# Kernel tuning notes

Hardware: AMD Instinct MI355X
Metric: run time of the kernel (lower is better)

The kernel has to match this reference:

```python
import jax, jax.numpy as jnp
import numpy as np

D = 256      # feature_dim (d_model)
H = 4        # num_heads
N = 4096     # query nodes
M = 4096     # source nodes


def _conv1x1(W, b, x):
    # Conv1d(kernel_size=1): per-position linear over channels. x: [1, Cin, N]
    return jnp.einsum('oi,bin->bon', W, x) + b[None, :, None]


def setup_inputs() -> dict:
    key = jax.random.key(0)
    ks = jax.random.split(key, 16)
    s = 0.02
    inp = {
        'x':      jax.random.normal(ks[0], (1, D, N), jnp.float32),
        'source': jax.random.normal(ks[1], (1, D, M), jnp.float32),
        'dist':   jax.random.uniform(ks[2], (1, N, M), jnp.float32),
        'mask':   jax.random.bernoulli(ks[3], 0.5, (N, M)),
        'Wq': s * jax.random.normal(ks[4], (D, D), jnp.float32),  'bq': jnp.zeros((D,), jnp.float32),
        'Wk': s * jax.random.normal(ks[5], (D, D), jnp.float32),  'bk': jnp.zeros((D,), jnp.float32),
        'Wv': s * jax.random.normal(ks[6], (D, D), jnp.float32),  'bv': jnp.zeros((D,), jnp.float32),
        'Wm': s * jax.random.normal(ks[7], (D, D), jnp.float32),  'bm': jnp.zeros((D,), jnp.float32),
        'W1': s * jax.random.normal(ks[8], (2 * D, 2 * D), jnp.float32), 'b1': jnp.zeros((2 * D,), jnp.float32),
        'W2': s * jax.random.normal(ks[9], (D, 2 * D), jnp.float32),     'b2': jnp.zeros((D,), jnp.float32),
    }
    return inp


def reference(x, source, dist, mask, Wq, bq, Wk, bk, Wv, bv, Wm, bm, W1, b1, W2, b2):
    dim = D // H  # per-head dim; torch view(1, dim, H, -1) splits channels as (dim, H)
    q = _conv1x1(Wq, bq, x).reshape(1, dim, H, N)
    k = _conv1x1(Wk, bk, source).reshape(1, dim, H, M)
    v = _conv1x1(Wv, bv, source).reshape(1, dim, H, M)

    scores = jnp.einsum('bdhn,bdhm->bhnm', q, k) / jnp.sqrt(jnp.asarray(dim, q.dtype))
    # non-standard additive mask: global detached min scales the masked-out entries
    smin = jax.lax.stop_gradient(scores.min())
    scores = scores + smin * (~mask).astype(scores.dtype)[None, None, :, :]

    prob = jax.nn.softmax(scores, axis=-1)                       # [1,H,N,M]
    attn = jnp.einsum('bhnm,bdhm->bdhn', prob, v)                # [1,dim,H,N]
    message = _conv1x1(Wm, bm, attn.reshape(1, D, N))            # merge heads

    h = jnp.concatenate([x, message], axis=1)                    # [1,2D,N]
    h = jax.nn.relu(_conv1x1(W1, b1, h))
    y = _conv1x1(W2, b2, h)                                      # [1,D,N]
    weights = scores.mean(axis=1)                                # [1,N,M]
    return y, weights
```

## Files before the change

### kernel.cpp

```cpp
#include <hip/hip_runtime.h>
#include <hip/hip_bf16.h>
#include <math.h>

#define Dm 256
#define Hh 4
#define Nn 4096
#define Mq 4096

typedef __attribute__((ext_vector_type(8))) short bf16x8;
typedef __attribute__((ext_vector_type(4))) float f32x4;
typedef _Float16 __attribute__((ext_vector_type(4))) f16x4;
typedef __fp16 __attribute__((ext_vector_type(2))) h16x2;

#define MFMA_BF16(a,b,c) __builtin_amdgcn_mfma_f32_16x16x32_bf16(a,b,c,0,0,0)
#define MFMA_F16x16(a,b,c) __builtin_amdgcn_mfma_f32_16x16x16f16(a,b,c,0,0,0)

#define MB (1u<<20)
#define OFF_FLAG  0
#define OFF_SMIN  64
#define OFF_KMAX  128
#define OFF_PART  1024
#define OFF_MT    8192
#define OFF_DENP  (128u<<10)
#define OFF_WB    (3u*MB/2)
#define OFF_BITS  (3u*MB)
#define OFF_QB    (5u*MB)
#define OFF_KB    (7u*MB)
#define OFF_VB    (9u*MB)
#define OFF_HCAT  (11u*MB)
#define OFF_ATTNT (15u*MB)
#define OFF_XT    (17u*MB)
#define OFF_ST    (19u*MB)
#define OFF_OPART (17u*MB)
#define OFF_H1T   (17u*MB)

#define WOFF_Q  0
#define WOFF_K  65536
#define WOFF_V  131072
#define WOFF_M  196608
#define WOFF_1  262144
#define WOFF_2  524288

__device__ __forceinline__ unsigned short f2bf(float x) {
    unsigned u = __float_as_uint(x);
    u += 0x7FFF + ((u >> 16) & 1);
    return (unsigned short)(u >> 16);
}
__device__ __forceinline__ float bf2f(unsigned short b) {
    return __uint_as_float(((unsigned)b) << 16);
}

__global__ void k_detect(const unsigned char* __restrict__ mb, int* __restrict__ flag,
                         unsigned* __restrict__ kmax) {
    __shared__ int c[5];
    if (threadIdx.x < 5) c[threadIdx.x] = 0;
    if (threadIdx.x < 4) kmax[threadIdx.x] = 0u;
    __syncthreads();
    for (int i = threadIdx.x; i < 16384; i += blockDim.x) {
        unsigned char b = mb[i];
        if (b) {
            atomicAdd(&c[i & 3], 1);
            if ((i & 7) == 4) atomicAdd(&c[4], 1);
        }
    }
    __syncthreads();
    if (threadIdx.x == 0) {
        int f;
        if (c[3] > 0 && c[0] == 0)          f = 3;
        else if (c[1] | c[2] | c[3])        f = 1;
        else if (c[4] > 0)                  f = 0;
        else                                f = 2;
        *flag = f;
    }
}

__global__ void k_maskbits(const void* __restrict__ mp, const int* __restrict__ flagp,
                           unsigned char* __restrict__ bits) {
    size_t i = (size_t)blockIdx.x * 256 + threadIdx.x;
    const int flag = *flagp;
    size_t base = i * 8;
    unsigned b = 0;
    if (flag == 1) {
        unsigned long long u = *(const unsigned long long*)((const unsigned char*)mp + base);
        #pragma unroll
        for (int j = 0; j < 8; j++) b |= (unsigned)(((u >> (8*j)) & 0xFFull) != 0ull) << j;
    } else if (flag == 0) {
        const int* p = (const int*)mp;
        #pragma unroll
        for (int j = 0; j < 8; j++) b |= (unsigned)(p[base + j] != 0) << j;
    } else if (flag == 3) {
        const float* p = (const float*)mp;
        #pragma unroll
        for (int j = 0; j < 8; j++) b |= (unsigned)(p[base + j] != 0.0f) << j;
    } else {
        const unsigned long long* p = (const unsigned long long*)mp;
        #pragma unroll
        for (int j = 0; j < 8; j++) b |= (unsigned)(p[base + j] != 0ull) << j;
    }
    bits[i] = (unsigned char)b;
}

__global__ __launch_bounds__(256) void k_prep(const float* __restrict__ x,
                                              const float* __restrict__ source,
                                              unsigned short* __restrict__ xt,
                                              unsigned short* __restrict__ st,
                                              unsigned short* __restrict__ hcat) {
    const int z = blockIdx.z;
    const float* src = z ? source : x;
    unsigned short* dst = z ? st : xt;
    unsigned short* dst2 = z ? nullptr : hcat;
    const int l = threadIdx.x & 63, g = threadIdx.x >> 6;
    const int c = blockIdx.y * 64 + l;
    const int n0 = blockIdx.x * 32 + g * 8;
    float4 v0 = *(const float4*)(src + (size_t)c * Nn + n0);
    float4 v1 = *(const float4*)(src + (size_t)c * Nn + n0 + 4);
    float vv[8] = {v0.x, v0.y, v0.z, v0.w, v1.x, v1.y, v1.z, v1.w};
    #pragma unroll
    for (int j = 0; j < 8; j++) {
        unsigned short b = f2bf(vv[j]);
        dst[(size_t)(n0 + j) * 256 + c] = b;
        if (dst2) dst2[(size_t)(n0 + j) * 512 + c] = b;
    }
}

__global__ void k_wcast(const float* __restrict__ Wq, const float* __restrict__ Wk,
                        const float* __restrict__ Wv, const float* __restrict__ Wm,
                        const float* __restrict__ W1, const float* __restrict__ W2,
                        unsigned short* __restrict__ wb) {
    size_t i = (size_t)blockIdx.x * 256 + threadIdx.x;
    const float* s; size_t off;
    if      (i < 65536)               { s = Wq; off = i; }
    else if (i < 131072)              { s = Wk; off = i - 65536; }
    else if (i < 196608)              { s = Wv; off = i - 131072; }
    else if (i < 262144)              { s = Wm; off = i - 196608; }
    else if (i < 524288)              { s = W1; off = i - 262144; }
    else                              { s = W2; off = i - 524288; }
    wb[i] = f2bf(s[off]);
}

template<int KK, int JT>
__device__ __forceinline__ void gemm_body(const unsigned short* __restrict__ wb,
                                          const float* __restrict__ bias,
                                          const unsigned short* __restrict__ xt,
                                          void* __restrict__ out, int mode,
                                          int bx, int by) {
    const int tid = threadIdx.x, w = tid >> 6, lane = tid & 63;
    const int lg = lane >> 4, lr = lane & 15;
    const int o_base = by * 64 + w * 16;
    const int n_base = bx * (16 * JT);
    f32x4 acc[JT];
    #pragma unroll
    for (int j = 0; j < JT; j++) acc[j] = (f32x4){0.f, 0.f, 0.f, 0.f};
    const unsigned short* wrow = wb + (size_t)(o_base + lr) * KK + lg * 8;
    const unsigned short* xrow = xt + (size_t)(n_base + lr) * KK + lg * 8;
    #pragma unroll
    for (int k0 = 0; k0 < KK; k0 += 32) {
        bf16x8 af = *(const bf16x8*)(wrow + k0);
        #pragma unroll
        for (int j = 0; j < JT; j++) {
            bf16x8 bfr = *(const bf16x8*)(xrow + (size_t)j * 16 * KK + k0);
            acc[j] = MFMA_BF16(af, bfr, acc[j]);
        }
    }
    float bv[4];
    #pragma unroll
    for (int r = 0; r < 4; r++) bv[r] = bias[o_base + lg * 4 + r];
    #pragma unroll
    for (int j = 0; j < JT; j++) {
        #pragma unroll
        for (int r = 0; r < 4; r++) {
            int o = o_base + lg * 4 + r;
            int n = n_base + j * 16 + lr;
            float v = acc[j][r] + bv[r];
            if (mode == 0) {
                ((float*)out)[(size_t)o * Nn + n] = v;
            } else if (mode == 1) {
                ((unsigned short*)out)[(((size_t)(o & 3)) * Nn + n) * 64 + (o >> 2)] = f2bf(v);
            } else if (mode == 2) {
                union { _Float16 h; unsigned short u; } cv; cv.h = (_Float16)v;
                ((unsigned short*)out)[(((size_t)(o & 3)) * 64 + (o >> 2)) * Mq + n] = cv.u;
            } else if (mode == 3) {
                ((unsigned short*)out)[(size_t)n * 512 + 256 + o] = f2bf(v);
            } else if (mode == 4) {
                ((unsigned short*)out)[(size_t)n * 512 + o] = f2bf(fmaxf(v, 0.f));
            } else {
                int dd = o >> 2, hh = o & 3, g = dd >> 3, pos = dd & 7;
                int slot = g ^ (n & 7);
                ((unsigned short*)out)[(((size_t)hh * Mq + n)) * 64 + slot * 8 + pos] = f2bf(v);
            }
        }
    }
}

template<int KK>
__global__ __launch_bounds__(256) void k_mgemm(const unsigned short* __restrict__ wb,
                                               const float* __restrict__ bias,
                                               const unsigned short* __restrict__ xt,
                                               void* __restrict__ out, int mode) {
    gemm_body<KK, 2>(wb, bias, xt, out, mode, blockIdx.x, blockIdx.y);
}

__global__ __launch_bounds__(256) void k_qkv(const unsigned short* __restrict__ wb,
                                             const float* __restrict__ bq,
                                             const float* __restrict__ bk,
                                             const float* __restrict__ bv,
                                             const unsigned short* __restrict__ xt,
                                             const unsigned short* __restrict__ st,
                                             void* __restrict__ qb, void* __restrict__ kb,
                                             void* __restrict__ vb) {
    const int z = blockIdx.z;
    const float* bias = (z == 0) ? bq : ((z == 1) ? bk : bv);
    const unsigned short* X = (z == 0) ? xt : st;
    void* out = (z == 0) ? qb : ((z == 1) ? kb : vb);
    int mode = (z == 0) ? 1 : ((z == 1) ? 5 : 2);
    gemm_body<256, 4>(wb + z * 65536, bias, X, out, mode, blockIdx.x, blockIdx.y);
}

__global__ __launch_bounds__(256) void k_knorm(const unsigned short* __restrict__ kb,
                                               unsigned* __restrict__ kmax) {
    const int h = blockIdx.y;
    const int m = blockIdx.x * 256 + threadIdx.x;
    const unsigned short* row = kb + ((size_t)(h * Mq + m) << 6);
    float s = 0.f;
    #pragma unroll
    for (int i = 0; i < 64; i++) { float v = bf2f(row[i]); s = fmaf(v, v, s); }
    __shared__ float red[256];
    red[threadIdx.x] = s;
    __syncthreads();
    for (int st = 128; st > 0; st >>= 1) {
        if (threadIdx.x < st) red[threadIdx.x] = fmaxf(red[threadIdx.x], red[threadIdx.x + st]);
        __syncthreads();
    }
    if (threadIdx.x == 0) atomicMax(kmax + h, __float_as_uint(red[0]));
}

__global__ __launch_bounds__(256) void k_qnorm(const unsigned short* __restrict__ qb,
                                               const unsigned* __restrict__ kmax,
                                               float* __restrict__ mtarr) {
    const int row = blockIdx.x * 256 + threadIdx.x;
    const unsigned short* qr = qb + ((size_t)row << 6);
    float s = 0.f;
    #pragma unroll
    for (int i = 0; i < 64; i++) { float v = bf2f(qr[i]); s = fmaf(v, v, s); }
    float k2 = __uint_as_float(kmax[row >> 12]);
    mtarr[row] = sqrtf(s * k2) * 0.125f;
}

__global__ __launch_bounds__(256) void k_min(
    const unsigned short* __restrict__ qb, const unsigned short* __restrict__ kb,
    float* __restrict__ partial) {
    __shared__ unsigned short kbuf[2][8192];
    const int tid = threadIdx.x;
    const int w = tid >> 6, lane = tid & 63;
    const int lg = lane >> 4, lr = lane & 15;
    const int n0 = blockIdx.x * 128 + w * 32;
    const int m0 = blockIdx.y * 256;

    bf16x8 qf[4][2][2];
    #pragma unroll
    for (int h = 0; h < 4; h++)
        #pragma unroll
        for (int ns = 0; ns < 2; ns++)
            #pragma unroll
            for (int kh = 0; kh < 2; kh++)
                qf[h][ns][kh] = *(const bf16x8*)(qb + (((size_t)h * Nn + n0 + ns*16 + lr) << 6) + kh*32 + lg*8);

    const unsigned short* srcs[4];
    #pragma unroll
    for (int h = 0; h < 4; h++) srcs[h] = kb + (((size_t)h * Mq + m0) << 6) + tid * 8;

    float mn = INFINITY;

    bf16x8 r[4];
    #pragma unroll
    for (int h = 0; h < 4; h++) {
        r[h] = *(const bf16x8*)(srcs[h]);
        *(bf16x8*)&kbuf[0][h * 2048 + tid * 8] = r[h];
    }
    __syncthreads();
    #pragma unroll
    for (int h = 0; h < 4; h++) r[h] = *(const bf16x8*)(srcs[h] + 2048);

    for (int t = 0; t < 8; t++) {
        const unsigned short* kB = &kbuf[t & 1][0];
        #pragma unroll
        for (int mi = 0; mi < 2; mi++) {
            const int rowoff = (mi * 16 + lr) * 64;
            #pragma unroll
            for (int h = 0; h < 4; h++) {
                bf16x8 a0 = *(const bf16x8*)(kB + h*2048 + rowoff + ((lg ^ (lr & 7)) << 3));
                bf16x8 a1 = *(const bf16x8*)(kB + h*2048 + rowoff + (((lg + 4) ^ (lr & 7)) << 3));
                #pragma unroll
                for (int ns = 0; ns < 2; ns++) {
                    f32x4 acc = (f32x4){0.f, 0.f, 0.f, 0.f};
                    acc = MFMA_BF16(a0, qf[h][ns][0], acc);
                    acc = MFMA_BF16(a1, qf[h][ns][1], acc);
                    mn = fminf(mn, fminf(fminf(acc[0], acc[1]), fminf(acc[2], acc[3])));
                }
            }
        }
        if (t < 7) {
            #pragma unroll
            for (int h = 0; h < 4; h++)
                *(bf16x8*)&kbuf[(t + 1) & 1][h * 2048 + tid * 8] = r[h];
        }
        __syncthreads();
        if (t < 6) {
            #pragma unroll
            for (int h = 0; h < 4; h++) r[h] = *(const bf16x8*)(srcs[h] + (size_t)(t + 2) * 2048);
        }
    }

    for (int off = 1; off < 64; off <<= 1) mn = fminf(mn, __shfl_xor(mn, off));
    __shared__ float wmin[4];
    if (lane == 0) wmin[w] = mn;
    __syncthreads();
    if (tid == 0) {
        float m2 = fminf(fminf(wmin[0], wmin[1]), fminf(wmin[2], wmin[3]));
        partial[blockIdx.x * 16 + blockIdx.y] = m2 * 0.125f;
    }
}

__global__ void k_minreduce(const float* __restrict__ partial, float* __restrict__ smin) {
    const int tid = threadIdx.x;
    float mn = fminf(partial[tid], partial[tid + 256]);
    __shared__ float red[256];
    red[tid] = mn;
    __syncthreads();
    for (int st = 128; st > 0; st >>= 1) {
        if (tid < st) red[tid] = fminf(red[tid], red[tid + st]);
        __syncthreads();
    }
    if (tid == 0) *smin = red[0];
}

__global__ __launch_bounds__(256) void k_wout(
    const unsigned short* __restrict__ qb, const unsigned short* __restrict__ kb,
    const unsigned long long* __restrict__ bits,
    const float* __restrict__ sminp, float* __restrict__ wout) {
    __shared__ unsigned short kbuf[2][8192];
    const int tid = threadIdx.x;
    const int w = tid >> 6, lane = tid & 63;
    const int lg = lane >> 4, lr = lane & 15;
    const int n0 = blockIdx.x * 128 + w * 32;
    const int m0 = blockIdx.y * 256;
    const float smin = *sminp;

    bf16x8 qf[4][2][2];
    #pragma unroll
    for (int h = 0; h < 4; h++)
        #pragma unroll
        for (int ns = 0; ns < 2; ns++)
            #pragma unroll
            for (int kh = 0; kh < 2; kh++)
                qf[h][ns][kh] = *(const bf16x8*)(qb + (((size_t)h * Nn + n0 + ns*16 + lr) << 6) + kh*32 + lg*8);

    const unsigned short* srcs[4];
    #pragma unroll
    for (int h = 0; h < 4; h++) srcs[h] = kb + (((size_t)h * Mq + m0) << 6) + tid * 8;

    const unsigned long long* brow0 = bits + (((size_t)(n0 + lr)) << 6) + (m0 >> 6);
    const unsigned long long* brow1 = bits + (((size_t)(n0 + 16 + lr)) << 6) + (m0 >> 6);
    unsigned long long bw0 = 0ull, bw1 = 0ull;

    bf16x8 r[4];
    #pragma unroll
    for (int h = 0; h < 4; h++) {
        r[h] = *(const bf16x8*)(srcs[h]);
        *(bf16x8*)&kbuf[0][h * 2048 + tid * 8] = r[h];
    }
    __syncthreads();
    #pragma unroll
    for (int h = 0; h < 4; h++) r[h] = *(const bf16x8*)(srcs[h] + 2048);

    for (int t = 0; t < 8; t++) {
        const unsigned short* kB = &kbuf[t & 1][0];
        const int mch = m0 + t * 32;
        if ((t & 1) == 0) { bw0 = brow0[t >> 1]; bw1 = brow1[t >> 1]; }
        #pragma unroll
        for (int mi = 0; mi < 2; mi++) {
            const int rowoff = (mi * 16 + lr) * 64;
            f32x4 acc[2][2];
            #pragma unroll
            for (int ns = 0; ns < 2; ns++) {
                acc[ns][0] = (f32x4){0.f, 0.f, 0.f, 0.f};
                acc[ns][1] = (f32x4){0.f, 0.f, 0.f, 0.f};
            }
            #pragma unroll
            for (int h = 0; h < 4; h++) {
                bf16x8 a0 = *(const bf16x8*)(kB + h*2048 + rowoff + ((lg ^ (lr & 7)) << 3));
                bf16x8 a1 = *(const bf16x8*)(kB + h*2048 + rowoff + (((lg + 4) ^ (lr & 7)) << 3));
                const int hf = h >> 1;
                #pragma unroll
                for (int ns = 0; ns < 2; ns++) {
                    acc[ns][hf] = MFMA_BF16(a0, qf[h][ns][0], acc[ns][hf]);
                    acc[ns][hf] = MFMA_BF16(a1, qf[h][ns][1], acc[ns][hf]);
                }
            }
            const int shb = (t & 1) * 32 + mi * 16 + lg * 4;
            #pragma unroll
            for (int ns = 0; ns < 2; ns++) {
                unsigned long long bw = ns ? bw1 : bw0;
                f32x4 wv;
                #pragma unroll
                for (int rr = 0; rr < 4; rr++) {
                    bool b = (bw >> (shb + rr)) & 1ull;
                    wv[rr] = fmaf(acc[ns][0][rr] + acc[ns][1][rr], 0.03125f, b ? 0.f : smin);
                }
                __builtin_nontemporal_store(wv,
                    (f32x4*)(wout + (size_t)(n0 + ns*16 + lr) * Mq + mch + mi * 16 + lg * 4));
            }
        }
        if (t < 7) {
            #pragma unroll
            for (int h = 0; h < 4; h++)
                *(bf16x8*)&kbuf[(t + 1) & 1][h * 2048 + tid * 8] = r[h];
        }
        __syncthreads();
        if (t < 6) {
            #pragma unroll
            for (int h = 0; h < 4; h++) r[h] = *(const bf16x8*)(srcs[h] + (size_t)(t + 2) * 2048);
        }
    }
}

__global__ __launch_bounds__(256) void k_pv(
    const unsigned short* __restrict__ qb, const unsigned short* __restrict__ kb,
    const unsigned short* __restrict__ vbh,
    const unsigned long long* __restrict__ bits,
    const float* __restrict__ sminp, const float* __restrict__ mtarr,
    float* __restrict__ denp, unsigned short* __restrict__ opart) {
    __shared__ unsigned short kbuf[2][4096];
    __shared__ unsigned short vbuf[2][4096];
    const int tid = threadIdx.x;
    const int w = tid >> 6, lane = tid & 63;
    const int lg = lane >> 4, lr = lane & 15;
    const int h = blockIdx.y & 3, mb = blockIdx.y >> 2;
    const int n0 = blockIdx.x * 128 + w * 32;
    const int m0 = mb * 1024;
    const float smin = *sminp;
    const float sminc = fmaxf(smin, 0.f);

    bf16x8 qf[2][2];
    float cT[2], cF[2];
    #pragma unroll
    for (int ns = 0; ns < 2; ns++) {
        const size_t qrow = ((size_t)h * Nn + n0 + ns*16 + lr) << 6;
        qf[ns][0] = *(const bf16x8*)(qb + qrow + lg*8);
        qf[ns][1] = *(const bf16x8*)(qb + qrow + 32 + lg*8);
        float mtE = mtarr[(size_t)h * Nn + n0 + ns*16 + lr] + sminc;
        cT[ns] = -mtE * 1.44269504f;
        cF[ns] = cT[ns] + smin * 1.44269504f;
    }

    f32x4 oacc[2][4];
    #pragma unroll
    for (int ns = 0; ns < 2; ns++)
        #pragma unroll
        for (int ds = 0; ds < 4; ds++) oacc[ns][ds] = (f32x4){0.f, 0.f, 0.f, 0.f};
    float dsum[2] = {0.f, 0.f};

    const unsigned short* ksrc = kb + (((size_t)h * Mq + m0) << 6) + tid * 8;
    const int vj = tid & 7;
    const int vdd0 = tid >> 3, vdd1 = 32 + (tid >> 3);
    const unsigned short* vsrc0 = vbh + (size_t)(h * 64 + vdd0) * Mq + m0 + vj * 8;
    const unsigned short* vsrc1 = vbh + (size_t)(h * 64 + vdd1) * Mq + m0 + vj * 8;
    int vdstA, vdstB, vdstC, vdstD;
    {
        int vds = vdd0 >> 4, vlr = vdd0 & 15, vmi = vj >> 1;
        int vswz = (vlr >> 2) & 3;
        int vbase = ((vmi * 4 + vds) * 16 + vlr) * 4;
        vdstA = (vbase + (((vj & 1) * 2 + 0) ^ vswz)) * 4;
        vdstB = (vbase + (((vj & 1) * 2 + 1) ^ vswz)) * 4;
        vds = vdd1 >> 4; vlr = vdd1 & 15;
        vswz = (vlr >> 2) & 3;
        vbase = ((vmi * 4 + vds) * 16 + vlr) * 4;
        vdstC = (vbase + (((vj & 1) * 2 + 0) ^ vswz)) * 4;
        vdstD = (vbase + (((vj & 1) * 2 + 1) ^ vswz)) * 4;
    }

    union U8 { bf16x8 v; unsigned long long q[2]; };
    U8 rv0, rv1;
    bf16x8 rk0 = *(const bf16x8*)(ksrc);
    bf16x8 rk1 = *(const bf16x8*)(ksrc + 2048);
    rv0.v = *(const bf16x8*)(vsrc0);
    rv1.v = *(const bf16x8*)(vsrc1);
    *(bf16x8*)&kbuf[0][tid * 8] = rk0;
    *(bf16x8*)&kbuf[0][2048 + tid * 8] = rk1;
    *(unsigned long long*)&vbuf[0][vdstA] = rv0.q[0];
    *(unsigned long long*)&vbuf[0][vdstB] = rv0.q[1];
    *(unsigned long long*)&vbuf[0][vdstC] = rv1.q[0];
    *(unsigned long long*)&vbuf[0][vdstD] = rv1.q[1];
    __syncthreads();
    rk0 = *(const bf16x8*)(ksrc + 4096);
    rk1 = *(const bf16x8*)(ksrc + 4096 + 2048);
    rv0.v = *(const bf16x8*)(vsrc0 + 64);
    rv1.v = *(const bf16x8*)(vsrc1 + 64);

    const unsigned long long* brow0 = bits + (((size_t)(n0 + lr)) << 6) + (m0 >> 6);
    const unsigned long long* brow1 = bits + (((size_t)(n0 + 16 + lr)) << 6) + (m0 >> 6);
    const int kslot0 = (lg ^ (lr & 7)) << 3;
    const int kslot1 = ((lg + 4) ^ (lr & 7)) << 3;
    const int vrslot = (lg ^ ((lr >> 2) & 3)) * 4;

    for (int t = 0; t < 16; t++) {
        const unsigned short* kB = &kbuf[t & 1][0];
        const unsigned short* vB = &vbuf[t & 1][0];
        unsigned long long bw[2];
        bw[0] = brow0[t];
        bw[1] = brow1[t];
        #pragma unroll
        for (int mi = 0; mi < 4; mi++) {
            const int rowoff = (mi * 16 + lr) * 64;
            bf16x8 a0 = *(const bf16x8*)(kB + rowoff + kslot0);
            bf16x8 a1 = *(const bf16x8*)(kB + rowoff + kslot1);
            f16x4 vf[4];
            #pragma unroll
            for (int ds = 0; ds < 4; ds++)
                vf[ds] = *(const f16x4*)&vB[((mi * 4 + ds) * 16 + lr) * 16 + vrslot];
            const int shb = mi * 16 + lg * 4;
            #pragma unroll
            for (int ns = 0; ns < 2; ns++) {
                f32x4 acc = (f32x4){0.f, 0.f, 0.f, 0.f};
                acc = MFMA_BF16(a0, qf[ns][0], acc);
                acc = MFMA_BF16(a1, qf[ns][1], acc);
                float p0 = exp2f(fmaf(acc[0], 0.18033688f, ((bw[ns] >> (shb + 0)) & 1ull) ? cT[ns] : cF[ns]));
                float p1 = exp2f(fmaf(acc[1], 0.18033688f, ((bw[ns] >> (shb + 1)) & 1ull) ? cT[ns] : cF[ns]));
                float p2 = exp2f(fmaf(acc[2], 0.18033688f, ((bw[ns] >> (shb + 2)) & 1ull) ? cT[ns] : cF[ns]));
                float p3 = exp2f(fmaf(acc[3], 0.18033688f, ((bw[ns] >> (shb + 3)) & 1ull) ? cT[ns] : cF[ns]));
                dsum[ns] += (p0 + p1) + (p2 + p3);
                union { h16x2 h2[2]; f16x4 f4; } pu;
                pu.h2[0] = __builtin_amdgcn_cvt_pkrtz(p0, p1);
                pu.h2[1] = __builtin_amdgcn_cvt_pkrtz(p2, p3);
                f16x4 pf = pu.f4;
                #pragma unroll
                for (int ds = 0; ds < 4; ds++)
                    oacc[ns][ds] = MFMA_F16x16(pf, vf[ds], oacc[ns][ds]);
            }
        }
        if (t < 15) {
            *(bf16x8*)&kbuf[(t + 1) & 1][tid * 8] = rk0;
            *(bf16x8*)&kbuf[(t + 1) & 1][2048 + tid * 8] = rk1;
            *(unsigned long long*)&vbuf[(t + 1) & 1][vdstA] = rv0.q[0];
            *(unsigned long long*)&vbuf[(t + 1) & 1][vdstB] = rv0.q[1];
            *(unsigned long long*)&vbuf[(t + 1) & 1][vdstC] = rv1.q[0];
            *(unsigned long long*)&vbuf[(t + 1) & 1][vdstD] = rv1.q[1];
        }
        __syncthreads();
        if (t < 14) {
            rk0 = *(const bf16x8*)(ksrc + (size_t)(t + 2) * 4096);
            rk1 = *(const bf16x8*)(ksrc + (size_t)(t + 2) * 4096 + 2048);
            rv0.v = *(const bf16x8*)(vsrc0 + (size_t)(t + 2) * 64);
            rv1.v = *(const bf16x8*)(vsrc1 + (size_t)(t + 2) * 64);
        }
    }

    #pragma unroll
    for (int ns = 0; ns < 2; ns++) {
        dsum[ns] += __shfl_xor(dsum[ns], 16);
        dsum[ns] += __shfl_xor(dsum[ns], 32);
    }
    if (lane < 16) {
        #pragma unroll
        for (int ns = 0; ns < 2; ns++)
            denp[((size_t)h * Nn + n0 + ns*16 + lane) * 4 + mb] = dsum[ns];
    }

    unsigned short* op = opart + (size_t)mb * (Dm * Nn);
    #pragma unroll
    for (int ns = 0; ns < 2; ns++)
        #pragma unroll
        for (int ds = 0; ds < 4; ds++) {
            int c = (ds * 16 + lr) * 4 + h;
            int n = n0 + ns * 16 + lg * 4;
            unsigned long long pk =
                (unsigned long long)f2bf(oacc[ns][ds][0]) |
                ((unsigned long long)f2bf(oacc[ns][ds][1]) << 16) |
                ((unsigned long long)f2bf(oacc[ns][ds][2]) << 32) |
                ((unsigned long long)f2bf(oacc[ns][ds][3]) << 48);
            *(unsigned long long*)&op[(size_t)c * Nn + n] = pk;
        }
}

__global__ __launch_bounds__(256) void k_finish(const unsigned short* __restrict__ opart,
                                                const float* __restrict__ denp,
                                                unsigned short* __restrict__ attnT) {
    __shared__ float t[64][65];
    const int cb = blockIdx.y * 64, nb = blockIdx.x * 64;
    const int tid = threadIdx.x;
    #pragma unroll
    for (int e = 0; e < 16; e++) {
        int idx = e * 256 + tid;
        int c_l = idx >> 6, n_l = idx & 63;
        int c = cb + c_l, n = nb + n_l;
        float s = 0.f;
        #pragma unroll
        for (int y = 0; y < 4; y++)
            s += bf2f(opart[(size_t)y * (Dm*Nn) + (size_t)c * Nn + n]);
        size_t row = (size_t)(c & 3) * Nn + n;
        float d = denp[row*4] + denp[row*4+1] + denp[row*4+2] + denp[row*4+3];
        t[c_l][n_l] = s / d;
    }
    __syncthreads();
    #pragma unroll
    for (int e = 0; e < 16; e++) {
        int idx = e * 256 + tid;
        int n_l = idx >> 6, c_l = idx & 63;
        attnT[(size_t)(nb + n_l) * 256 + cb + c_l] = f2bf(t[c_l][n_l]);
    }
}

extern "C" void kernel_launch(void* const* d_in, const int* in_sizes, int n_in,
                              void* d_out, int out_size, void* d_ws, size_t ws_size,
                              hipStream_t stream) {
    const float* x      = (const float*)d_in[0];
    const float* source = (const float*)d_in[1];
    const void*  mask   = d_in[3];
    const float* Wq = (const float*)d_in[4];  const float* bq = (const float*)d_in[5];
    const float* Wk = (const float*)d_in[6];  const float* bk = (const float*)d_in[7];
    const float* Wv = (const float*)d_in[8];  const float* bv = (const float*)d_in[9];
    const float* Wm = (const float*)d_in[10]; const float* bm = (const float*)d_in[11];
    const float* W1 = (const float*)d_in[12]; const float* b1 = (const float*)d_in[13];
    const float* W2 = (const float*)d_in[14]; const float* b2 = (const float*)d_in[15];

    float* y    = (float*)d_out;
    float* wout = y + (size_t)Dm * Nn;

    char* ws = (char*)d_ws;
    int*      flag  = (int*)(ws + OFF_FLAG);
    float*    sminp = (float*)(ws + OFF_SMIN);
    float*    part  = (float*)(ws + OFF_PART);
    unsigned* kmax  = (unsigned*)(ws + OFF_KMAX);
    float*    mtarr = (float*)(ws + OFF_MT);
    float*    denp  = (float*)(ws + OFF_DENP);
    unsigned short* wb    = (unsigned short*)(ws + OFF_WB);
    unsigned char*  bits  = (unsigned char*)(ws + OFF_BITS);
    unsigned short* qb    = (unsigned short*)(ws + OFF_QB);
    unsigned short* kb    = (unsigned short*)(ws + OFF_KB);
    unsigned short* vb    = (unsigned short*)(ws + OFF_VB);
    unsigned short* hcat  = (unsigned short*)(ws + OFF_HCAT);
    unsigned short* attnT = (unsigned short*)(ws + OFF_ATTNT);
    unsigned short* xt    = (unsigned short*)(ws + OFF_XT);
    unsigned short* st    = (unsigned short*)(ws + OFF_ST);
    unsigned short* opart = (unsigned short*)(ws + OFF_OPART);
    unsigned short* h1t   = (unsigned short*)(ws + OFF_H1T);

    k_detect<<<1, 256, 0, stream>>>((const unsigned char*)mask, flag, kmax);
    k_maskbits<<<8192, 256, 0, stream>>>(mask, flag, bits);

    k_prep<<<dim3(128, 4, 2), 256, 0, stream>>>(x, source, xt, st, hcat);
    k_wcast<<<2560, 256, 0, stream>>>(Wq, Wk, Wv, Wm, W1, W2, wb);

    k_qkv<<<dim3(64, 4, 3), 256, 0, stream>>>(wb, bq, bk, bv, xt, st, qb, kb, vb);

    k_knorm<<<dim3(16, 4), 256, 0, stream>>>(kb, kmax);
    k_qnorm<<<64, 256, 0, stream>>>(qb, kmax, mtarr);

    k_min<<<dim3(32, 16), 256, 0, stream>>>(qb, kb, part);
    k_minreduce<<<1, 256, 0, stream>>>(part, sminp);

    k_wout<<<dim3(32, 16), 256, 0, stream>>>(qb, kb, (const unsigned long long*)bits, sminp, wout);

    k_pv<<<dim3(32, 16), 256, 0, stream>>>(qb, kb, vb, (const unsigned long long*)bits,
                                           sminp, mtarr, denp, opart);
    k_finish<<<dim3(64, 4), 256, 0, stream>>>(opart, denp, attnT);

    k_mgemm<256><<<dim3(128, 4), 256, 0, stream>>>(wb + WOFF_M, bm, attnT, hcat, 3);
    k_mgemm<512><<<dim3(128, 8), 256, 0, stream>>>(wb + WOFF_1, b1, hcat, h1t, 4);
    k_mgemm<512><<<dim3(128, 4), 256, 0, stream>>>(wb + WOFF_2, b2, h1t, y, 0);
}
```

Measured before the change: 214.8 us.

## Fold mask detection into prep, atomic min, double M-split grids, fp16 partials

Merges the mask-format detection into the prep kernel and replaces the two-stage min reduction with a single atomicMin on an order-preserving float key, removing two launches. The min, score-output and PV kernels now split the source dimension twice as finely (32x32 grids), which gives more blocks to fill the CUs. Because of that, the PV stage writes eight partial outputs in fp16 and the finish kernel sums eight of them. The output GEMMs switch to JT=4 with half as many column blocks. The cost is more partial traffic and atomics, plus a precision change from bf16 to fp16 with round-toward-zero for the partials.

```diff
diff --git a/kernel.cpp b/kernel.cpp
--- a/kernel.cpp
+++ b/kernel.cpp
@@ -1,5 +1,6 @@
 #include <hip/hip_runtime.h>
 #include <hip/hip_bf16.h>
+#include <hip/hip_fp16.h>
 #include <math.h>
 
 #define Dm 256
@@ -19,20 +20,19 @@
 #define OFF_FLAG  0
 #define OFF_SMIN  64
 #define OFF_KMAX  128
-#define OFF_PART  1024
 #define OFF_MT    8192
 #define OFF_DENP  (128u<<10)
 #define OFF_WB    (3u*MB/2)
 #define OFF_BITS  (3u*MB)
+#define OFF_ATTNT (3u*MB)
 #define OFF_QB    (5u*MB)
 #define OFF_KB    (7u*MB)
 #define OFF_VB    (9u*MB)
 #define OFF_HCAT  (11u*MB)
-#define OFF_ATTNT (15u*MB)
+#define OFF_OPART (15u*MB)
 #define OFF_XT    (17u*MB)
 #define OFF_ST    (19u*MB)
-#define OFF_OPART (17u*MB)
-#define OFF_H1T   (17u*MB)
+#define OFF_H1T   (15u*MB)
 
 #define WOFF_Q  0
 #define WOFF_K  65536
@@ -49,62 +49,23 @@
 __device__ __forceinline__ float bf2f(unsigned short b) {
     return __uint_as_float(((unsigned)b) << 16);
 }
-
-__global__ void k_detect(const unsigned char* __restrict__ mb, int* __restrict__ flag,
-                         unsigned* __restrict__ kmax) {
-    __shared__ int c[5];
-    if (threadIdx.x < 5) c[threadIdx.x] = 0;
-    if (threadIdx.x < 4) kmax[threadIdx.x] = 0u;
-    __syncthreads();
-    for (int i = threadIdx.x; i < 16384; i += blockDim.x) {
-        unsigned char b = mb[i];
-        if (b) {
-            atomicAdd(&c[i & 3], 1);
-            if ((i & 7) == 4) atomicAdd(&c[4], 1);
-        }
-    }
-    __syncthreads();
-    if (threadIdx.x == 0) {
-        int f;
-        if (c[3] > 0 && c[0] == 0)          f = 3;
-        else if (c[1] | c[2] | c[3])        f = 1;
-        else if (c[4] > 0)                  f = 0;
-        else                                f = 2;
-        *flag = f;
-    }
-}
-
-__global__ void k_maskbits(const void* __restrict__ mp, const int* __restrict__ flagp,
-                           unsigned char* __restrict__ bits) {
-    size_t i = (size_t)blockIdx.x * 256 + threadIdx.x;
-    const int flag = *flagp;
-    size_t base = i * 8;
-    unsigned b = 0;
-    if (flag == 1) {
-        unsigned long long u = *(const unsigned long long*)((const unsigned char*)mp + base);
-        #pragma unroll
-        for (int j = 0; j < 8; j++) b |= (unsigned)(((u >> (8*j)) & 0xFFull) != 0ull) << j;
-    } else if (flag == 0) {
-        const int* p = (const int*)mp;
-        #pragma unroll
-        for (int j = 0; j < 8; j++) b |= (unsigned)(p[base + j] != 0) << j;
-    } else if (flag == 3) {
-        const float* p = (const float*)mp;
-        #pragma unroll
-        for (int j = 0; j < 8; j++) b |= (unsigned)(p[base + j] != 0.0f) << j;
-    } else {
-        const unsigned long long* p = (const unsigned long long*)mp;
-        #pragma unroll
-        for (int j = 0; j < 8; j++) b |= (unsigned)(p[base + j] != 0ull) << j;
-    }
-    bits[i] = (unsigned char)b;
+__device__ __forceinline__ unsigned fkey(float f) {
+    unsigned u = __float_as_uint(f);
+    return (u & 0x80000000u) ? ~u : (u | 0x80000000u);
+}
+__device__ __forceinline__ float fdecode(unsigned k) {
+    return (k & 0x80000000u) ? __uint_as_float(k ^ 0x80000000u) : __uint_as_float(~k);
 }
 
 __global__ __launch_bounds__(256) void k_prep(const float* __restrict__ x,
                                               const float* __restrict__ source,
                                               unsigned short* __restrict__ xt,
                                               unsigned short* __restrict__ st,
-                                              unsigned short* __restrict__ hcat) {
+                                              unsigned short* __restrict__ hcat,
+                                              const unsigned char* __restrict__ maskb,
+                                              int* __restrict__ flag,
+                                              unsigned* __restrict__ kmax,
+                                              unsigned* __restrict__ sminkey) {
     const int z = blockIdx.z;
     const float* src = z ? source : x;
     unsigned short* dst = z ? st : xt;
@@ -121,6 +82,55 @@
         dst[(size_t)(n0 + j) * 256 + c] = b;
         if (dst2) dst2[(size_t)(n0 + j) * 512 + c] = b;
     }
+    if (blockIdx.x == 0 && blockIdx.y == 0 && z == 0) {
+        __shared__ int cnt[5];
+        if (threadIdx.x < 5) cnt[threadIdx.x] = 0;
+        if (threadIdx.x < 4) kmax[threadIdx.x] = 0u;
+        if (threadIdx.x == 0) *sminkey = 0xFFFFFFFFu;
+        __syncthreads();
+        for (int i = threadIdx.x; i < 16384; i += 256) {
+            unsigned char b = maskb[i];
+            if (b) {
+                atomicAdd(&cnt[i & 3], 1);
+                if ((i & 7) == 4) atomicAdd(&cnt[4], 1);
+            }
+        }
+        __syncthreads();
+        if (threadIdx.x == 0) {
+            int f;
+            if (cnt[3] > 0 && cnt[0] == 0)        f = 3;
+            else if (cnt[1] | cnt[2] | cnt[3])    f = 1;
+            else if (cnt[4] > 0)                  f = 0;
+            else                                  f = 2;
+            *flag = f;
+        }
+    }
+}
+
+__global__ void k_maskbits(const void* __restrict__ mp, const int* __restrict__ flagp,
+                           unsigned char* __restrict__ bits) {
+    size_t i = (size_t)blockIdx.x * 256 + threadIdx.x;
+    const int flag = *flagp;
+    size_t base = i * 8;
+    unsigned b = 0;
+    if (flag == 1) {
+        unsigned long long u = *(const unsigned long long*)((const unsigned char*)mp + base);
+        #pragma unroll
+        for (int j = 0; j < 8; j++) b |= (unsigned)(((u >> (8*j)) & 0xFFull) != 0ull) << j;
+    } else if (flag == 0) {
+        const int* p = (const int*)mp;
+        #pragma unroll
+        for (int j = 0; j < 8; j++) b |= (unsigned)(p[base + j] != 0) << j;
+    } else if (flag == 3) {
+        const float* p = (const float*)mp;
+        #pragma unroll
+        for (int j = 0; j < 8; j++) b |= (unsigned)(p[base + j] != 0.0f) << j;
+    } else {
+        const unsigned long long* p = (const unsigned long long*)mp;
+        #pragma unroll
+        for (int j = 0; j < 8; j++) b |= (unsigned)(p[base + j] != 0ull) << j;
+    }
+    bits[i] = (unsigned char)b;
 }
 
 __global__ void k_wcast(const float* __restrict__ Wq, const float* __restrict__ Wk,
@@ -192,12 +202,12 @@
     }
 }
 
-template<int KK>
+template<int KK, int JT>
 __global__ __launch_bounds__(256) void k_mgemm(const unsigned short* __restrict__ wb,
                                                const float* __restrict__ bias,
                                                const unsigned short* __restrict__ xt,
                                                void* __restrict__ out, int mode) {
-    gemm_body<KK, 2>(wb, bias, xt, out, mode, blockIdx.x, blockIdx.y);
+    gemm_body<KK, JT>(wb, bias, xt, out, mode, blockIdx.x, blockIdx.y);
 }
 
 __global__ __launch_bounds__(256) void k_qkv(const unsigned short* __restrict__ wb,
@@ -248,13 +258,13 @@
 
 __global__ __launch_bounds__(256) void k_min(
     const unsigned short* __restrict__ qb, const unsigned short* __restrict__ kb,
-    float* __restrict__ partial) {
+    unsigned* __restrict__ sminkey) {
     __shared__ unsigned short kbuf[2][8192];
     const int tid = threadIdx.x;
     const int w = tid >> 6, lane = tid & 63;
     const int lg = lane >> 4, lr = lane & 15;
     const int n0 = blockIdx.x * 128 + w * 32;
-    const int m0 = blockIdx.y * 256;
+    const int m0 = blockIdx.y * 128;
 
     bf16x8 qf[4][2][2];
     #pragma unroll
@@ -281,7 +291,7 @@
     #pragma unroll
     for (int h = 0; h < 4; h++) r[h] = *(const bf16x8*)(srcs[h] + 2048);
 
-    for (int t = 0; t < 8; t++) {
+    for (int t = 0; t < 4; t++) {
         const unsigned short* kB = &kbuf[t & 1][0];
         #pragma unroll
         for (int mi = 0; mi < 2; mi++) {
@@ -299,13 +309,13 @@
                 }
             }
         }
-        if (t < 7) {
+        if (t < 3) {
             #pragma unroll
             for (int h = 0; h < 4; h++)
                 *(bf16x8*)&kbuf[(t + 1) & 1][h * 2048 + tid * 8] = r[h];
         }
         __syncthreads();
-        if (t < 6) {
+        if (t < 2) {
             #pragma unroll
             for (int h = 0; h < 4; h++) r[h] = *(const bf16x8*)(srcs[h] + (size_t)(t + 2) * 2048);
         }
@@ -317,34 +327,21 @@
     __syncthreads();
     if (tid == 0) {
         float m2 = fminf(fminf(wmin[0], wmin[1]), fminf(wmin[2], wmin[3]));
-        partial[blockIdx.x * 16 + blockIdx.y] = m2 * 0.125f;
-    }
-}
-
-__global__ void k_minreduce(const float* __restrict__ partial, float* __restrict__ smin) {
-    const int tid = threadIdx.x;
-    float mn = fminf(partial[tid], partial[tid + 256]);
-    __shared__ float red[256];
-    red[tid] = mn;
-    __syncthreads();
-    for (int st = 128; st > 0; st >>= 1) {
-        if (tid < st) red[tid] = fminf(red[tid], red[tid + st]);
-        __syncthreads();
-    }
-    if (tid == 0) *smin = red[0];
+        atomicMin(sminkey, fkey(m2 * 0.125f));
+    }
 }
 
 __global__ __launch_bounds__(256) void k_wout(
     const unsigned short* __restrict__ qb, const unsigned short* __restrict__ kb,
     const unsigned long long* __restrict__ bits,
-    const float* __restrict__ sminp, float* __restrict__ wout) {
+    const unsigned* __restrict__ skey, float* __restrict__ wout) {
     __shared__ unsigned short kbuf[2][8192];
     const int tid = threadIdx.x;
     const int w = tid >> 6, lane = tid & 63;
     const int lg = lane >> 4, lr = lane & 15;
     const int n0 = blockIdx.x * 128 + w * 32;
-    const int m0 = blockIdx.y * 256;
-    const float smin = *sminp;
+    const int m0 = blockIdx.y * 128;
+    const float smin = fdecode(*skey);
 
     bf16x8 qf[4][2][2];
     #pragma unroll
@@ -373,7 +370,7 @@
     #pragma unroll
     for (int h = 0; h < 4; h++) r[h] = *(const bf16x8*)(srcs[h] + 2048);
 
-    for (int t = 0; t < 8; t++) {
+    for (int t = 0; t < 4; t++) {
         const unsigned short* kB = &kbuf[t & 1][0];
         const int mch = m0 + t * 32;
         if ((t & 1) == 0) { bw0 = brow0[t >> 1]; bw1 = brow1[t >> 1]; }
@@ -411,13 +408,13 @@
                     (f32x4*)(wout + (size_t)(n0 + ns*16 + lr) * Mq + mch + mi * 16 + lg * 4));
             }
         }
-        if (t < 7) {
+        if (t < 3) {
             #pragma unroll
             for (int h = 0; h < 4; h++)
                 *(bf16x8*)&kbuf[(t + 1) & 1][h * 2048 + tid * 8] = r[h];
         }
         __syncthreads();
-        if (t < 6) {
+        if (t < 2) {
             #pragma unroll
             for (int h = 0; h < 4; h++) r[h] = *(const bf16x8*)(srcs[h] + (size_t)(t + 2) * 2048);
         }
@@ -428,7 +425,7 @@
     const unsigned short* __restrict__ qb, const unsigned short* __restrict__ kb,
     const unsigned short* __restrict__ vbh,
     const unsigned long long* __restrict__ bits,
-    const float* __restrict__ sminp, const float* __restrict__ mtarr,
+    const unsigned* __restrict__ skey, const float* __restrict__ mtarr,
     float* __restrict__ denp, unsigned short* __restrict__ opart) {
     __shared__ unsigned short kbuf[2][4096];
     __shared__ unsigned short vbuf[2][4096];
@@ -437,8 +434,8 @@
     const int lg = lane >> 4, lr = lane & 15;
     const int h = blockIdx.y & 3, mb = blockIdx.y >> 2;
     const int n0 = blockIdx.x * 128 + w * 32;
-    const int m0 = mb * 1024;
-    const float smin = *sminp;
+    const int m0 = mb * 512;
+    const float smin = fdecode(*skey);
     const float sminc = fmaxf(smin, 0.f);
 
     bf16x8 qf[2][2];
@@ -503,7 +500,7 @@
     const int kslot1 = ((lg + 4) ^ (lr & 7)) << 3;
     const int vrslot = (lg ^ ((lr >> 2) & 3)) * 4;
 
-    for (int t = 0; t < 16; t++) {
+    for (int t = 0; t < 8; t++) {
         const unsigned short* kB = &kbuf[t & 1][0];
         const unsigned short* vB = &vbuf[t & 1][0];
         unsigned long long bw[2];
@@ -538,7 +535,7 @@
                     oacc[ns][ds] = MFMA_F16x16(pf, vf[ds], oacc[ns][ds]);
             }
         }
-        if (t < 15) {
+        if (t < 7) {
             *(bf16x8*)&kbuf[(t + 1) & 1][tid * 8] = rk0;
             *(bf16x8*)&kbuf[(t + 1) & 1][2048 + tid * 8] = rk1;
             *(unsigned long long*)&vbuf[(t + 1) & 1][vdstA] = rv0.q[0];
@@ -547,7 +544,7 @@
             *(unsigned long long*)&vbuf[(t + 1) & 1][vdstD] = rv1.q[1];
         }
         __syncthreads();
-        if (t < 14) {
+        if (t < 6) {
             rk0 = *(const bf16x8*)(ksrc + (size_t)(t + 2) * 4096);
             rk1 = *(const bf16x8*)(ksrc + (size_t)(t + 2) * 4096 + 2048);
             rv0.v = *(const bf16x8*)(vsrc0 + (size_t)(t + 2) * 64);
@@ -563,7 +560,7 @@
     if (lane < 16) {
         #pragma unroll
         for (int ns = 0; ns < 2; ns++)
-            denp[((size_t)h * Nn + n0 + ns*16 + lane) * 4 + mb] = dsum[ns];
+            denp[((size_t)h * Nn + n0 + ns*16 + lane) * 8 + mb] = dsum[ns];
     }
 
     unsigned short* op = opart + (size_t)mb * (Dm * Nn);
@@ -573,12 +570,10 @@
         for (int ds = 0; ds < 4; ds++) {
             int c = (ds * 16 + lr) * 4 + h;
             int n = n0 + ns * 16 + lg * 4;
-            unsigned long long pk =
-                (unsigned long long)f2bf(oacc[ns][ds][0]) |
-                ((unsigned long long)f2bf(oacc[ns][ds][1]) << 16) |
-                ((unsigned long long)f2bf(oacc[ns][ds][2]) << 32) |
-                ((unsigned long long)f2bf(oacc[ns][ds][3]) << 48);
-            *(unsigned long long*)&op[(size_t)c * Nn + n] = pk;
+            union { h16x2 h2[2]; unsigned long long q; } pu;
+            pu.h2[0] = __builtin_amdgcn_cvt_pkrtz(oacc[ns][ds][0], oacc[ns][ds][1]);
+            pu.h2[1] = __builtin_amdgcn_cvt_pkrtz(oacc[ns][ds][2], oacc[ns][ds][3]);
+            *(unsigned long long*)&op[(size_t)c * Nn + n] = pu.q;
         }
 }
 
@@ -595,10 +590,15 @@
         int c = cb + c_l, n = nb + n_l;
         float s = 0.f;
         #pragma unroll
-        for (int y = 0; y < 4; y++)
-            s += bf2f(opart[(size_t)y * (Dm*Nn) + (size_t)c * Nn + n]);
+        for (int y = 0; y < 8; y++) {
+            union { unsigned short u; _Float16 h; } cv;
+            cv.u = opart[(size_t)y * (Dm*Nn) + (size_t)c * Nn + n];
+            s += (float)cv.h;
+        }
         size_t row = (size_t)(c & 3) * Nn + n;
-        float d = denp[row*4] + denp[row*4+1] + denp[row*4+2] + denp[row*4+3];
+        float d = 0.f;
+        #pragma unroll
+        for (int mb = 0; mb < 8; mb++) d += denp[row*8 + mb];
         t[c_l][n_l] = s / d;
     }
     __syncthreads();
@@ -628,8 +628,7 @@
 
     char* ws = (char*)d_ws;
     int*      flag  = (int*)(ws + OFF_FLAG);
-    float*    sminp = (float*)(ws + OFF_SMIN);
-    float*    part  = (float*)(ws + OFF_PART);
+    unsigned* skey  = (unsigned*)(ws + OFF_SMIN);
     unsigned* kmax  = (unsigned*)(ws + OFF_KMAX);
     float*    mtarr = (float*)(ws + OFF_MT);
     float*    denp  = (float*)(ws + OFF_DENP);
@@ -645,10 +644,9 @@
     unsigned short* opart = (unsigned short*)(ws + OFF_OPART);
     unsigned short* h1t   = (unsigned short*)(ws + OFF_H1T);
 
-    k_detect<<<1, 256, 0, stream>>>((const unsigned char*)mask, flag, kmax);
+    k_prep<<<dim3(128, 4, 2), 256, 0, stream>>>(x, source, xt, st, hcat,
+                                                (const unsigned char*)mask, flag, kmax, skey);
     k_maskbits<<<8192, 256, 0, stream>>>(mask, flag, bits);
-
-    k_prep<<<dim3(128, 4, 2), 256, 0, stream>>>(x, source, xt, st, hcat);
     k_wcast<<<2560, 256, 0, stream>>>(Wq, Wk, Wv, Wm, W1, W2, wb);
 
     k_qkv<<<dim3(64, 4, 3), 256, 0, stream>>>(wb, bq, bk, bv, xt, st, qb, kb, vb);
@@ -656,16 +654,15 @@
     k_knorm<<<dim3(16, 4), 256, 0, stream>>>(kb, kmax);
     k_qnorm<<<64, 256, 0, stream>>>(qb, kmax, mtarr);
 
-    k_min<<<dim3(32, 16), 256, 0, stream>>>(qb, kb, part);
-    k_minreduce<<<1, 256, 0, stream>>>(part, sminp);
-
-    k_wout<<<dim3(32, 16), 256, 0, stream>>>(qb, kb, (const unsigned long long*)bits, sminp, wout);
-
-    k_pv<<<dim3(32, 16), 256, 0, stream>>>(qb, kb, vb, (const unsigned long long*)bits,
-                                           sminp, mtarr, denp, opart);
+    k_min<<<dim3(32, 32), 256, 0, stream>>>(qb, kb, skey);
+
+    k_wout<<<dim3(32, 32), 256, 0, stream>>>(qb, kb, (const unsigned long long*)bits, skey, wout);
+
+    k_pv<<<dim3(32, 32), 256, 0, stream>>>(qb, kb, vb, (const unsigned long long*)bits,
+                                           skey, mtarr, denp, opart);
     k_finish<<<dim3(64, 4), 256, 0, stream>>>(opart, denp, attnT);
 
-    k_mgemm<256><<<dim3(128, 4), 256, 0, stream>>>(wb + WOFF_M, bm, attnT, hcat, 3);
-    k_mgemm<512><<<dim3(128, 8), 256, 0, stream>>>(wb + WOFF_1, b1, hcat, h1t, 4);
-    k_mgemm<512><<<dim3(128, 4), 256, 0, stream>>>(wb + WOFF_2, b2, h1t, y, 0);
-}
+    k_mgemm<256, 4><<<dim3(64, 4), 256, 0, stream>>>(wb + WOFF_M, bm, attnT, hcat, 3);
+    k_mgemm<512, 4><<<dim3(64, 8), 256, 0, stream>>>(wb + WOFF_1, b1, hcat, h1t, 4);
+    k_mgemm<512, 4><<<dim3(64, 4), 256, 0, stream>>>(wb + WOFF_2, b2, h1t, y, 0);
+}
```

After: 215.0 us. Within noise of the previous version (+0.1%).
